# Optimization experiments

Hardware: AMD Instinct MI355X
Metric: run time of the kernel (lower is better)

The kernel has to match this reference:

```python
import jax, jax.numpy as jnp
import numpy as np

K = 5  # Chebyshev order


def laplacian(w):
    # normalized Laplacian: I - D^{-1/2} W D^{-1/2}
    d = jnp.sum(w, axis=1)
    d_re = 1.0 / jnp.sqrt(d + 1e-5)
    return jnp.eye(w.shape[0], dtype=w.dtype) - d_re[:, None] * w * d_re[None, :]


def cheb_terms(x, lap, k):
    # x: [B,N,C], lap: [N,N] -> [B,k,N,C]
    # Faithful to torch code: T0 = ones, then (x, lap@x) recurrence for k>2.
    t0 = jnp.ones_like(x)
    if k == 1:
        return t0[:, None]
    t1 = jnp.matmul(lap, x)
    if k == 2:
        return jnp.stack([t0, t1], axis=1)
    terms = [t0, x, t1]
    tkm1, tk = x, t1
    for _ in range(3, k):
        tkm1, tk = tk, 2.0 * jnp.matmul(lap, tk) - tkm1
        terms.append(tk)
    return jnp.stack(terms, axis=1)


def graph_conv(x, lap, w, k):
    # torch: cp.permute(0,2,3,1).flatten(2) @ w, i.e. flat index = c*k + t
    t = cheb_terms(x, lap, k)                       # [B,k,N,C]
    C = x.shape[-1]
    O = w.shape[-1]
    return jnp.einsum('bknc,cko->bno', t, w.reshape(C, k, O))


def setup_inputs() -> dict:
    key = jax.random.key(0)
    ks = jax.random.split(key, 9)
    B, N, Cin, H = 8192, 32, 60, 128
    return {
        'x': jax.random.normal(ks[0], (B, N, Cin), dtype=jnp.float32),
        'adj': jax.random.normal(ks[1], (N, N), dtype=jnp.float32) * 0.1,
        'adj_bias': jax.random.normal(ks[2], (1,), dtype=jnp.float32) * 0.1 + 0.2,
        'w1': jax.random.normal(ks[3], (K * Cin, H), dtype=jnp.float32) * 0.05,
        'b1': jax.random.normal(ks[4], (1, 1, H), dtype=jnp.float32) * 0.05,
        'w2': jax.random.normal(ks[5], (K * H, H), dtype=jnp.float32) * 0.05,
        'b2': jax.random.normal(ks[6], (1, 1, H), dtype=jnp.float32) * 0.05,
        'fc_w': jax.random.normal(ks[7], (2, N * H), dtype=jnp.float32) * 0.02,
        'fc_b': jax.random.normal(ks[8], (2,), dtype=jnp.float32) * 0.02,
    }


def reference(x, adj, adj_bias, w1, b1, w2, b2, fc_w, fc_b):
    # DGCNN.forward (eval mode: dropout = identity)
    a = jax.nn.relu(adj + adj_bias)
    lap = laplacian(a)
    h = graph_conv(x, lap, w1, K)
    h = jax.nn.relu(h + b1)      # B1ReLU
    h = graph_conv(h, lap, w2, K)
    h = jax.nn.relu(h + b2)
    h = h.reshape(h.shape[0], -1)  # [B, N*H]
    return h @ fc_w.T + fc_b
```

## Files before the change

### kernel.cpp

```cpp
#include <hip/hip_runtime.h>

typedef unsigned short u16;
typedef unsigned int u32;
typedef short bf16x8 __attribute__((ext_vector_type(8)));
typedef float f32x4 __attribute__((ext_vector_type(4)));
typedef u32 u32x4 __attribute__((ext_vector_type(4)));

#define MFMA16(a, b, c) __builtin_amdgcn_mfma_f32_16x16x32_bf16((a), (b), (c), 0, 0, 0)

__device__ __forceinline__ u16 f2bf(float f) {
  u32 u = __builtin_bit_cast(u32, f);
  u += 0x7FFFu + ((u >> 16) & 1u);
  return (u16)(u >> 16);
}
__device__ __forceinline__ u32 pk2bf(float a, float b) {
  u32 ua = __builtin_bit_cast(u32, a) + 0x8000u;
  u32 ub = __builtin_bit_cast(u32, b) + 0x8000u;
  return (ua >> 16) | (ub & 0xFFFF0000u);
}

#define WS_MGF   0
#define WS_WT1F  8192
#define WS_WT2F  73728
#define WS_B1    204800
#define WS_B2    205312

__global__ void prep_kernel(const float* __restrict__ adj,
                            const float* __restrict__ adj_bias,
                            const float* __restrict__ w1,
                            const float* __restrict__ b1,
                            const float* __restrict__ w2,
                            const float* __restrict__ b2,
                            char* __restrict__ ws) {
  const int tid = threadIdx.x;
  if (blockIdx.x == 0) {
    __shared__ float sa[1024], Ls[1024], L2s[1024], L3s[1024], sdre[32];
    float bias = adj_bias[0];
    for (int i = tid; i < 1024; i += 256) sa[i] = fmaxf(adj[i] + bias, 0.0f);
    __syncthreads();
    if (tid < 32) {
      float s = 0.0f;
      for (int c = 0; c < 32; ++c) s += sa[tid * 32 + c];
      sdre[tid] = 1.0f / sqrtf(s + 1e-5f);
    }
    __syncthreads();
    for (int i = tid; i < 1024; i += 256) {
      int n = i >> 5, c = i & 31;
      Ls[i] = (n == c ? 1.0f : 0.0f) - sdre[n] * sa[i] * sdre[c];
    }
    __syncthreads();
    for (int i = tid; i < 1024; i += 256) {
      int r = i >> 5, c = i & 31;
      float s = 0.0f;
      for (int m = 0; m < 32; ++m) s += Ls[r * 32 + m] * Ls[m * 32 + c];
      L2s[i] = s;
    }
    __syncthreads();
    for (int i = tid; i < 1024; i += 256) {
      int r = i >> 5, c = i & 31;
      float s = 0.0f;
      for (int m = 0; m < 32; ++m) s += L2s[r * 32 + m] * Ls[m * 32 + c];
      L3s[i] = s;
    }
    __syncthreads();
    u16* MGf = (u16*)(ws + WS_MGF);
    for (int i = tid; i < 4096; i += 256) {
      int jt = i >> 9, lane = (i >> 3) & 63, j = i & 7;
      int col = jt * 16 + (lane & 15);
      int k = ((lane >> 4) << 3) + j;
      int kk = col >> 5, np = col & 31;
      float v;
      if (kk == 0)      v = (np == k) ? 1.0f : 0.0f;
      else if (kk == 1) v = Ls[np * 32 + k];
      else if (kk == 2) v = 2.0f * L2s[np * 32 + k] - (np == k ? 1.0f : 0.0f);
      else              v = 4.0f * L3s[np * 32 + k] - 3.0f * Ls[np * 32 + k];
      MGf[i] = f2bf(v);
    }
    float* B1 = (float*)(ws + WS_B1);
    float* B2 = (float*)(ws + WS_B2);
    if (tid < 128) {
      float s = b1[tid];
      for (int c = 0; c < 60; ++c) s += w1[(c * 5) * 128 + tid];
      B1[tid] = s;
    } else {
      int o = tid - 128;
      float s = b2[o];
      for (int c = 0; c < 128; ++c) s += w2[(c * 5) * 128 + o];
      B2[o] = s;
    }
  } else {
    u16* WT1F = (u16*)(ws + WS_WT1F);
    u16* WT2F = (u16*)(ws + WS_WT2F);
    int g = (blockIdx.x - 1) * 256 + tid;
    for (int i = g; i < 32768; i += 16 * 256) {
      int j = i & 7, lane = (i >> 3) & 63, ks = (i >> 9) & 3;
      int h = (i >> 11) & 1, ot = i >> 12;
      int q = lane >> 4;
      int c = h * 32 + ((j >> 2) << 4) + q * 4 + (j & 3);
      int o = ot * 16 + (lane & 15);
      WT1F[i] = (c < 60) ? f2bf(w1[(c * 5 + ks + 1) * 128 + o]) : (u16)0;
    }
    for (int i = g; i < 65536; i += 16 * 256) {
      int j = i & 7, lane = (i >> 3) & 63, ks = (i >> 9) & 3;
      int h = (i >> 11) & 3, mt = i >> 13;
      int q = lane >> 4;
      int c2 = h * 32 + ((j >> 2) << 4) + q * 4 + (j & 3);
      int o = mt * 16 + (lane & 15);
      WT2F[i] = f2bf(w2[(c2 * 5 + ks + 1) * 128 + o]);
    }
  }
}

__global__ __launch_bounds__(256, 4) void dgcnn_kernel(
    const float* __restrict__ x,
    const char* __restrict__ ws,
    const float* __restrict__ fc_w,
    const float* __restrict__ fc_b,
    float* __restrict__ out) {
  __shared__ __align__(16) char arena[32768];
  u16* XtA = (u16*)arena;
  u16* XtB = (u16*)(arena + 5120);
  u16* HtA = (u16*)arena;
  u16* HtB = (u16*)(arena + 8192);
  u16* YA  = (u16*)(arena + 16384);
  u16* YB  = (u16*)(arena + 24576);
  float* red = (float*)arena;

  const u16* MGf  = (const u16*)(ws + WS_MGF);
  const u16* WT1F = (const u16*)(ws + WS_WT1F);
  const u16* WT2F = (const u16*)(ws + WS_WT2F);
  const float* bias1 = (const float*)(ws + WS_B1);
  const float* bias2 = (const float*)(ws + WS_B2);

  const int tid = threadIdx.x;
  const int w = tid >> 6, lane = tid & 63;
  const int l15 = lane & 15, q = lane >> 4;
  const int b0 = blockIdx.x * 2;
  const f32x4 z4 = {0.0f, 0.0f, 0.0f, 0.0f};

  bf16x8 mB0 = *(const bf16x8*)(MGf + ((2 * w + 0) * 64 + lane) * 8);
  bf16x8 mB1 = *(const bf16x8*)(MGf + ((2 * w + 1) * 64 + lane) * 8);

  const float* xb = x + (size_t)b0 * 1920;
  {
    int tn = (tid & 15) * 2;
    int tc = (tid >> 4) * 4;
    if (tc < 60) {
      float4 a0 = *(const float4*)(xb + tn * 60 + tc);
      float4 a1 = *(const float4*)(xb + tn * 60 + 60 + tc);
      float4 c0 = *(const float4*)(xb + 1920 + tn * 60 + tc);
      float4 c1 = *(const float4*)(xb + 1920 + tn * 60 + 60 + tc);
      *(u32*)&XtA[(tc + 0) * 40 + tn] = pk2bf(a0.x, a1.x);
      *(u32*)&XtA[(tc + 1) * 40 + tn] = pk2bf(a0.y, a1.y);
      *(u32*)&XtA[(tc + 2) * 40 + tn] = pk2bf(a0.z, a1.z);
      *(u32*)&XtA[(tc + 3) * 40 + tn] = pk2bf(a0.w, a1.w);
      *(u32*)&XtB[(tc + 0) * 40 + tn] = pk2bf(c0.x, c1.x);
      *(u32*)&XtB[(tc + 1) * 40 + tn] = pk2bf(c0.y, c1.y);
      *(u32*)&XtB[(tc + 2) * 40 + tn] = pk2bf(c0.z, c1.z);
      *(u32*)&XtB[(tc + 3) * 40 + tn] = pk2bf(c0.w, c1.w);
    } else {
#pragma unroll
      for (int j = 0; j < 4; ++j) {
        *(u32*)&XtA[(tc + j) * 40 + tn] = 0;
        *(u32*)&XtB[(tc + j) * 40 + tn] = 0;
      }
    }
  }
  __syncthreads();

  const int ysw_w = ((w * 4 + q) ^ (l15 & 7)) * 8;
  const int psr = (q ^ (l15 & 3) ^ (l15 >> 2)) * 8;

  f32x4 gA00, gA01, gA10, gA11, gB00, gB01, gB10, gB11;
  u32x4 yA0, yA1, yB0, yB1;

  auto g1c_x = [&](int h) {
    int r0 = ((2 * h + 0) * 16 + l15) * 40 + q * 8;
    int r1 = ((2 * h + 1) * 16 + l15) * 40 + q * 8;
    bf16x8 aA0 = *(const bf16x8*)&XtA[r0];
    bf16x8 aA1 = *(const bf16x8*)&XtA[r1];
    bf16x8 aB0 = *(const bf16x8*)&XtB[r0];
    bf16x8 aB1 = *(const bf16x8*)&XtB[r1];
    gA00 = MFMA16(aA0, mB0, z4); gA01 = MFMA16(aA0, mB1, z4);
    gA10 = MFMA16(aA1, mB0, z4); gA11 = MFMA16(aA1, mB1, z4);
    gB00 = MFMA16(aB0, mB0, z4); gB01 = MFMA16(aB0, mB1, z4);
    gB10 = MFMA16(aB1, mB0, z4); gB11 = MFMA16(aB1, mB1, z4);
  };
  auto g1c_h = [&](int h) {
    int o20 = ((2 * h + 0) * 16 + l15) * 32 + psr;
    int o21 = ((2 * h + 1) * 16 + l15) * 32 + psr;
    bf16x8 aA0 = *(const bf16x8*)&HtA[o20];
    bf16x8 aA1 = *(const bf16x8*)&HtA[o21];
    bf16x8 aB0 = *(const bf16x8*)&HtB[o20];
    bf16x8 aB1 = *(const bf16x8*)&HtB[o21];
    gA00 = MFMA16(aA0, mB0, z4); gA01 = MFMA16(aA0, mB1, z4);
    gA10 = MFMA16(aA1, mB0, z4); gA11 = MFMA16(aA1, mB1, z4);
    gB00 = MFMA16(aB0, mB0, z4); gB01 = MFMA16(aB0, mB1, z4);
    gB10 = MFMA16(aB1, mB0, z4); gB11 = MFMA16(aB1, mB1, z4);
  };
  auto ypk = [&]() {
    yA0 = (u32x4){pk2bf(gA00[0], gA00[1]), pk2bf(gA00[2], gA00[3]),
                  pk2bf(gA10[0], gA10[1]), pk2bf(gA10[2], gA10[3])};
    yB0 = (u32x4){pk2bf(gB00[0], gB00[1]), pk2bf(gB00[2], gB00[3]),
                  pk2bf(gB10[0], gB10[1]), pk2bf(gB10[2], gB10[3])};
    yA1 = (u32x4){pk2bf(gA01[0], gA01[1]), pk2bf(gA01[2], gA01[3]),
                  pk2bf(gA11[0], gA11[1]), pk2bf(gA11[2], gA11[3])};
    yB1 = (u32x4){pk2bf(gB01[0], gB01[1]), pk2bf(gB01[2], gB01[3]),
                  pk2bf(gB11[0], gB11[1]), pk2bf(gB11[2], gB11[3])};
  };
  auto yst = [&]() {
    *(u32x4*)&YA[(0 * 16 + l15) * 128 + ysw_w] = yA0;
    *(u32x4*)&YB[(0 * 16 + l15) * 128 + ysw_w] = yB0;
    *(u32x4*)&YA[(1 * 16 + l15) * 128 + ysw_w] = yA1;
    *(u32x4*)&YB[(1 * 16 + l15) * 128 + ysw_w] = yB1;
  };

  f32x4 acc1A[2][2] = {{z4, z4}, {z4, z4}};
  f32x4 acc1B[2][2] = {{z4, z4}, {z4, z4}};
  auto einsum1 = [&](int h) {
    __builtin_amdgcn_s_setprio(1);
#pragma unroll
    for (int ks = 0; ks < 4; ++ks) {
      const u16* wp = WT1F + (size_t)((((2 * w) * 2 + h) * 4 + ks) * 64 + lane) * 8;
      bf16x8 wfa = *(const bf16x8*)wp;
      bf16x8 wfb = *(const bf16x8*)(wp + 4096);
      int ysw = ((ks * 4 + q) ^ (l15 & 7)) * 8;
      bf16x8 a0A = *(const bf16x8*)&YA[l15 * 128 + ysw];
      bf16x8 a1A = *(const bf16x8*)&YA[(16 + l15) * 128 + ysw];
      bf16x8 a0B = *(const bf16x8*)&YB[l15 * 128 + ysw];
      bf16x8 a1B = *(const bf16x8*)&YB[(16 + l15) * 128 + ysw];
      acc1A[0][0] = MFMA16(a0A, wfa, acc1A[0][0]);
      acc1A[0][1] = MFMA16(a0A, wfb, acc1A[0][1]);
      acc1A[1][0] = MFMA16(a1A, wfa, acc1A[1][0]);
      acc1A[1][1] = MFMA16(a1A, wfb, acc1A[1][1]);
      acc1B[0][0] = MFMA16(a0B, wfa, acc1B[0][0]);
      acc1B[0][1] = MFMA16(a0B, wfb, acc1B[0][1]);
      acc1B[1][0] = MFMA16(a1B, wfa, acc1B[1][0]);
      acc1B[1][1] = MFMA16(a1B, wfb, acc1B[1][1]);
    }
    __builtin_amdgcn_s_setprio(0);
  };

  g1c_x(0);
  ypk();
  yst();
  __syncthreads();
  g1c_x(1);
  ypk();
  einsum1(0);
  __syncthreads();
  yst();
  __syncthreads();
  einsum1(1);

#pragma unroll
  for (int ot = 0; ot < 2; ++ot) {
    int o = (2 * w + ot) * 16 + l15;
    float bv = bias1[o];
#pragma unroll
    for (int mt = 0; mt < 2; ++mt) {
      int ps = (mt * 2 + (q >> 1)) ^ (l15 & 3) ^ (l15 >> 2);
      int idx = o * 32 + ps * 8 + (q & 1) * 4;
      uint2 vA, vB;
      vA.x = pk2bf(fmaxf(acc1A[mt][ot][0] + bv, 0.0f), fmaxf(acc1A[mt][ot][1] + bv, 0.0f));
      vA.y = pk2bf(fmaxf(acc1A[mt][ot][2] + bv, 0.0f), fmaxf(acc1A[mt][ot][3] + bv, 0.0f));
      vB.x = pk2bf(fmaxf(acc1B[mt][ot][0] + bv, 0.0f), fmaxf(acc1B[mt][ot][1] + bv, 0.0f));
      vB.y = pk2bf(fmaxf(acc1B[mt][ot][2] + bv, 0.0f), fmaxf(acc1B[mt][ot][3] + bv, 0.0f));
      *(uint2*)&HtA[idx] = vA;
      *(uint2*)&HtB[idx] = vB;
    }
  }
  __syncthreads();

  f32x4 acc2A[2][2] = {{z4, z4}, {z4, z4}};
  f32x4 acc2B[2][2] = {{z4, z4}, {z4, z4}};
  auto einsum2 = [&](int h) {
    __builtin_amdgcn_s_setprio(1);
#pragma unroll
    for (int ks = 0; ks < 4; ++ks) {
      const u16* wp = WT2F + (size_t)((((2 * w) * 4 + h) * 4 + ks) * 64 + lane) * 8;
      bf16x8 wfa = *(const bf16x8*)wp;
      bf16x8 wfb = *(const bf16x8*)(wp + 8192);
      int ysw = ((ks * 4 + q) ^ (l15 & 7)) * 8;
      bf16x8 by0A = *(const bf16x8*)&YA[l15 * 128 + ysw];
      bf16x8 by1A = *(const bf16x8*)&YA[(16 + l15) * 128 + ysw];
      bf16x8 by0B = *(const bf16x8*)&YB[l15 * 128 + ysw];
      bf16x8 by1B = *(const bf16x8*)&YB[(16 + l15) * 128 + ysw];
      acc2A[0][0] = MFMA16(wfa, by0A, acc2A[0][0]);
      acc2A[0][1] = MFMA16(wfa, by1A, acc2A[0][1]);
      acc2A[1][0] = MFMA16(wfb, by0A, acc2A[1][0]);
      acc2A[1][1] = MFMA16(wfb, by1A, acc2A[1][1]);
      acc2B[0][0] = MFMA16(wfa, by0B, acc2B[0][0]);
      acc2B[0][1] = MFMA16(wfa, by1B, acc2B[0][1]);
      acc2B[1][0] = MFMA16(wfb, by0B, acc2B[1][0]);
      acc2B[1][1] = MFMA16(wfb, by1B, acc2B[1][1]);
    }
    __builtin_amdgcn_s_setprio(0);
  };

  g1c_h(0);
  ypk();
  yst();
  __syncthreads();
#pragma unroll
  for (int h = 1; h < 4; ++h) {
    g1c_h(h);
    ypk();
    einsum2(h - 1);
    __syncthreads();
    yst();
    __syncthreads();
  }
  einsum2(3);

  float p0A = 0.0f, p1A = 0.0f, p0B = 0.0f, p1B = 0.0f;
#pragma unroll
  for (int ot = 0; ot < 2; ++ot) {
    int ob = (2 * w + ot) * 16 + q * 4;
    float4 bv = *(const float4*)&bias2[ob];
#pragma unroll
    for (int nt = 0; nt < 2; ++nt) {
      int n = nt * 16 + l15;
      float4 w0 = *(const float4*)&fc_w[n * 128 + ob];
      float4 w1v = *(const float4*)&fc_w[4096 + n * 128 + ob];
      float hA0 = fmaxf(acc2A[ot][nt][0] + bv.x, 0.0f);
      float hA1 = fmaxf(acc2A[ot][nt][1] + bv.y, 0.0f);
      float hA2 = fmaxf(acc2A[ot][nt][2] + bv.z, 0.0f);
      float hA3 = fmaxf(acc2A[ot][nt][3] + bv.w, 0.0f);
      float hB0 = fmaxf(acc2B[ot][nt][0] + bv.x, 0.0f);
      float hB1 = fmaxf(acc2B[ot][nt][1] + bv.y, 0.0f);
      float hB2 = fmaxf(acc2B[ot][nt][2] + bv.z, 0.0f);
      float hB3 = fmaxf(acc2B[ot][nt][3] + bv.w, 0.0f);
      p0A = fmaf(hA0, w0.x, fmaf(hA1, w0.y, fmaf(hA2, w0.z, fmaf(hA3, w0.w, p0A))));
      p1A = fmaf(hA0, w1v.x, fmaf(hA1, w1v.y, fmaf(hA2, w1v.z, fmaf(hA3, w1v.w, p1A))));
      p0B = fmaf(hB0, w0.x, fmaf(hB1, w0.y, fmaf(hB2, w0.z, fmaf(hB3, w0.w, p0B))));
      p1B = fmaf(hB0, w1v.x, fmaf(hB1, w1v.y, fmaf(hB2, w1v.z, fmaf(hB3, w1v.w, p1B))));
    }
  }
#pragma unroll
  for (int off = 32; off >= 1; off >>= 1) {
    p0A += __shfl_xor(p0A, off);
    p1A += __shfl_xor(p1A, off);
    p0B += __shfl_xor(p0B, off);
    p1B += __shfl_xor(p1B, off);
  }
  if (lane == 0) {
    red[w * 4 + 0] = p0A;
    red[w * 4 + 1] = p1A;
    red[w * 4 + 2] = p0B;
    red[w * 4 + 3] = p1B;
  }
  __syncthreads();
  if (tid < 4) {
    float s = red[tid] + red[4 + tid] + red[8 + tid] + red[12 + tid] + fc_b[tid & 1];
    out[(b0 + (tid >> 1)) * 2 + (tid & 1)] = s;
  }
}

extern "C" void kernel_launch(void* const* d_in, const int* in_sizes, int n_in,
                              void* d_out, int out_size, void* d_ws, size_t ws_size,
                              hipStream_t stream) {
  const float* x        = (const float*)d_in[0];
  const float* adj      = (const float*)d_in[1];
  const float* adj_bias = (const float*)d_in[2];
  const float* w1       = (const float*)d_in[3];
  const float* b1       = (const float*)d_in[4];
  const float* w2       = (const float*)d_in[5];
  const float* b2       = (const float*)d_in[6];
  const float* fc_w     = (const float*)d_in[7];
  const float* fc_b     = (const float*)d_in[8];
  float* out = (float*)d_out;
  char* ws   = (char*)d_ws;

  prep_kernel<<<17, 256, 0, stream>>>(adj, adj_bias, w1, b1, w2, b2, ws);
  dgcnn_kernel<<<4096, 256, 0, stream>>>(x, ws, fc_w, fc_b, out);
}
```

Measured before the change: 173.9 us.

## Double-buffer Y staging in LDS to drop one barrier per pipeline step

Splits the Y shared-memory staging buffer into two alternating buffers, so each step's store of the next Chebyshev slice can overlap the einsum reading the previous one. This removes one __syncthreads per step in both graph-conv stages. LDS use rises from 32 KB to 48 KB and launch bounds drop from 4 to 3 blocks per CU, which lowers occupancy.

Measured after the change: 176.1 us. No clear change (+1.2%).

```diff
diff --git a/kernel.cpp b/kernel.cpp
--- a/kernel.cpp
+++ b/kernel.cpp
@@ -111,19 +111,21 @@
   }
 }
 
-__global__ __launch_bounds__(256, 4) void dgcnn_kernel(
+__global__ __launch_bounds__(256, 3) void dgcnn_kernel(
     const float* __restrict__ x,
     const char* __restrict__ ws,
     const float* __restrict__ fc_w,
     const float* __restrict__ fc_b,
     float* __restrict__ out) {
-  __shared__ __align__(16) char arena[32768];
+  __shared__ __align__(16) char arena[49152];
   u16* XtA = (u16*)arena;
   u16* XtB = (u16*)(arena + 5120);
   u16* HtA = (u16*)arena;
   u16* HtB = (u16*)(arena + 8192);
-  u16* YA  = (u16*)(arena + 16384);
-  u16* YB  = (u16*)(arena + 24576);
+  u16* Y0A = (u16*)(arena + 16384);
+  u16* Y0B = (u16*)(arena + 24576);
+  u16* Y1A = (u16*)(arena + 32768);
+  u16* Y1B = (u16*)(arena + 40960);
   float* red = (float*)arena;
 
   const u16* MGf  = (const u16*)(ws + WS_MGF);
@@ -208,7 +210,9 @@
     yB1 = (u32x4){pk2bf(gB01[0], gB01[1]), pk2bf(gB01[2], gB01[3]),
                   pk2bf(gB11[0], gB11[1]), pk2bf(gB11[2], gB11[3])};
   };
-  auto yst = [&]() {
+  auto yst = [&](int b) {
+    u16* YA = b ? Y1A : Y0A;
+    u16* YB = b ? Y1B : Y0B;
     *(u32x4*)&YA[(0 * 16 + l15) * 128 + ysw_w] = yA0;
     *(u32x4*)&YB[(0 * 16 + l15) * 128 + ysw_w] = yB0;
     *(u32x4*)&YA[(1 * 16 + l15) * 128 + ysw_w] = yA1;
@@ -217,7 +221,9 @@
 
   f32x4 acc1A[2][2] = {{z4, z4}, {z4, z4}};
   f32x4 acc1B[2][2] = {{z4, z4}, {z4, z4}};
-  auto einsum1 = [&](int h) {
+  auto einsum1 = [&](int h, int b) {
+    const u16* YA = b ? Y1A : Y0A;
+    const u16* YB = b ? Y1B : Y0B;
     __builtin_amdgcn_s_setprio(1);
 #pragma unroll
     for (int ks = 0; ks < 4; ++ks) {
@@ -243,15 +249,14 @@
 
   g1c_x(0);
   ypk();
-  yst();
+  yst(0);
   __syncthreads();
   g1c_x(1);
   ypk();
-  einsum1(0);
-  __syncthreads();
-  yst();
-  __syncthreads();
-  einsum1(1);
+  einsum1(0, 0);
+  yst(1);
+  __syncthreads();
+  einsum1(1, 1);
 
 #pragma unroll
   for (int ot = 0; ot < 2; ++ot) {
@@ -274,7 +279,9 @@
 
   f32x4 acc2A[2][2] = {{z4, z4}, {z4, z4}};
   f32x4 acc2B[2][2] = {{z4, z4}, {z4, z4}};
-  auto einsum2 = [&](int h) {
+  auto einsum2 = [&](int h, int b) {
+    const u16* YA = b ? Y1A : Y0A;
+    const u16* YB = b ? Y1B : Y0B;
     __builtin_amdgcn_s_setprio(1);
 #pragma unroll
     for (int ks = 0; ks < 4; ++ks) {
@@ -300,18 +307,17 @@
 
   g1c_h(0);
   ypk();
-  yst();
+  yst(0);
   __syncthreads();
 #pragma unroll
   for (int h = 1; h < 4; ++h) {
     g1c_h(h);
     ypk();
-    einsum2(h - 1);
-    __syncthreads();
-    yst();
-    __syncthreads();
-  }
-  einsum2(3);
+    einsum2(h - 1, (h - 1) & 1);
+    yst(h & 1);
+    __syncthreads();
+  }
+  einsum2(3, 1);
 
   float p0A = 0.0f, p1A = 0.0f, p0B = 0.0f, p1B = 0.0f;
 #pragma unroll
```
